# Optimization experiments

Hardware: AMD Instinct MI355X
Metric: run time of the kernel (lower is better)

Reference implementation:

```python
import jax, jax.numpy as jnp
import numpy as np

B, H, S, HD = 4, 16, 4096, 64
DIM = 2 * HD
NF = 9
LAMBDA_INIT = 0.01


def setup_inputs() -> dict:
    key = jax.random.key(0)
    ks = jax.random.split(key, 8)
    shape = (B, H, S, HD)
    Q_t = jax.random.normal(ks[0], shape, jnp.float32)
    Q_prime_t = jax.random.normal(ks[1], shape, jnp.float32)
    K_t = jax.random.normal(ks[2], shape, jnp.float32)
    K_prime_t = jax.random.normal(ks[3], shape, jnp.float32)
    V = jax.random.normal(ks[4], shape, jnp.float32)
    lambdas = jnp.full((NF,), LAMBDA_INIT, jnp.float32)
    # xavier_uniform for [NF, DIM] linear weights
    bound = float(np.sqrt(6.0 / (NF + DIM)))
    Wq = jax.random.uniform(ks[5], (NF, DIM), jnp.float32, -bound, bound)
    Wk = jax.random.uniform(ks[6], (NF, DIM), jnp.float32, -bound, bound)
    return {"Q_t": Q_t, "Q_prime_t": Q_prime_t, "K_t": K_t,
            "K_prime_t": K_prime_t, "V": V,
            "lambdas": lambdas, "Wq": Wq, "Wk": Wk}


def _ste_argmax_route(scores):
    # forward: hard one-hot; backward: softmax gradient (straight-through)
    idx = jnp.argmax(scores, axis=-1)
    one_hot = jax.nn.one_hot(idx, scores.shape[-1], dtype=scores.dtype)
    soft = jax.nn.softmax(scores, axis=-1)
    return one_hot + soft - jax.lax.stop_gradient(soft)


def _lambda_for(x, x_prime, W, lambdas):
    cat = jax.lax.stop_gradient(jnp.concatenate([x, x_prime], axis=-1))  # [B,H,S,2hd]
    scores = jnp.einsum('bshd,nd->bshn'.replace('s', 'x'), cat, W)  # placeholder
    return scores


def reference(Q_t, Q_prime_t, K_t, K_prime_t, V, lambdas, Wq, Wk):
    # routing scores (routers see detached inputs)
    Q_cat = jax.lax.stop_gradient(jnp.concatenate([Q_t, Q_prime_t], axis=-1))  # [B,H,S,2hd]
    K_cat = jax.lax.stop_gradient(jnp.concatenate([K_t, K_prime_t], axis=-1))
    q_scores = jnp.einsum('bhsd,nd->bhsn', Q_cat, Wq)
    k_scores = jnp.einsum('bhsd,nd->bhsn', K_cat, Wk)
    q_route = _ste_argmax_route(q_scores)  # [B,H,S,NF]
    k_route = _ste_argmax_route(k_scores)
    lambda_q = jnp.sum(q_route * lambdas, axis=-1, keepdims=True)  # [B,H,S,1]
    lambda_k = jnp.sum(k_route * lambdas, axis=-1, keepdims=True)
    Q_diff = Q_t - lambda_q * Q_prime_t
    K_diff = K_t - lambda_k * K_prime_t
    KV = jnp.einsum('bhsd,bhse->bhde', K_diff, V)   # [B,H,hd,hd]
    O = jnp.einsum('bhsd,bhde->bhse', Q_diff, KV)   # [B,H,S,hd]
    return O
```

## Files before the change

kernel.cpp:

```cpp
#include <hip/hip_runtime.h>


#define Sx 4096
#define HDx 64
#define NF 9
#define NHEAD 64
#define NCHK 32
#define SCK (Sx / NCHK)
#define NTK (SCK / 64)
#define NCHO 64
#define LROW 72

typedef __attribute__((ext_vector_type(8))) short bf16x8;
typedef __attribute__((ext_vector_type(4))) float f32x4;

__device__ __forceinline__ unsigned short f2bf(float f) {
    union { float f; unsigned u; } x; x.f = f;
    unsigned r = x.u + 0x7fffu + ((x.u >> 16) & 1u);
    return (unsigned short)(r >> 16);
}
__device__ __forceinline__ float bf2f(unsigned short b) {
    union { unsigned u; float f; } x; x.u = ((unsigned)b) << 16;
    return x.f;
}
__device__ __forceinline__ bf16x8 pack8(float4 a, float4 b) {
    bf16x8 r;
    r[0] = (short)f2bf(a.x); r[1] = (short)f2bf(a.y);
    r[2] = (short)f2bf(a.z); r[3] = (short)f2bf(a.w);
    r[4] = (short)f2bf(b.x); r[5] = (short)f2bf(b.y);
    r[6] = (short)f2bf(b.z); r[7] = (short)f2bf(b.w);
    return r;
}

__device__ __forceinline__ float route_lam(float v, int l15, const float* lam9) {
    int idx = l15;
#pragma unroll
    for (int m = 1; m < 16; m <<= 1) {
        float ov = __shfl_xor(v, m, 16);
        int   oi = __shfl_xor(idx, m, 16);
        bool take = (ov > v) || (ov == v && oi < idx);
        v = take ? ov : v; idx = take ? oi : idx;
    }
    return lam9[idx];
}

__device__ __forceinline__ float lam_bcast(float r0, float r1, float r2, float r3, int l15) {
    const int src = ((l15 >> 2) << 4) + l15;
    float t0 = __shfl(r0, src);
    float t1 = __shfl(r1, src);
    float t2 = __shfl(r2, src);
    float t3 = __shfl(r3, src);
    float lo = (l15 & 1) ? t1 : t0;
    float hi = (l15 & 1) ? t3 : t2;
    return (l15 & 2) ? hi : lo;
}

__global__ __launch_bounds__(256, 4) void kv_kernel(
    const float* __restrict__ Kt, const float* __restrict__ Kp,
    const float* __restrict__ V,  const float* __restrict__ lambdas,
    const float* __restrict__ Wk, float* __restrict__ KVt)
{
    __shared__ __align__(16) unsigned short kd_s[64][LROW];
    __shared__ float lam9[16];

    const int tid  = threadIdx.x;
    const int lane = tid & 63;
    const int wave = tid >> 6;
    const int l15  = lane & 15;
    const int q    = lane >> 4;
    const int head  = blockIdx.x & (NHEAD - 1);
    const int chunk = blockIdx.x >> 6;
    const size_t hbase = (size_t)head * Sx * HDx;
    const int sbase = chunk * SCK;
    const int myrow = wave * 16 + l15;

    if (tid < NF) lam9[tid] = lambdas[tid];

    bf16x8 wb[4];
#pragma unroll
    for (int h = 0; h < 4; ++h)
#pragma unroll
        for (int j = 0; j < 8; ++j) {
            float w = (l15 < NF) ? Wk[l15 * 128 + h * 32 + q * 8 + j] : 0.f;
            wb[h][j] = (short)f2bf(w);
        }

    f32x4 acc[4];
#pragma unroll
    for (int mt = 0; mt < 4; ++mt) acc[mt] = (f32x4){0.f, 0.f, 0.f, 0.f};

    const float* kt0 = Kt + hbase + (size_t)(sbase + myrow) * HDx + q * 8;
    const float* kp0 = Kp + hbase + (size_t)(sbase + myrow) * HDx + q * 8;
    float4 a0 = *(const float4*)(kt0),      a1 = *(const float4*)(kt0 + 4);
    float4 a2 = *(const float4*)(kt0 + 32), a3 = *(const float4*)(kt0 + 36);
    float4 b0 = *(const float4*)(kp0),      b1 = *(const float4*)(kp0 + 4);
    float4 b2 = *(const float4*)(kp0 + 32), b3 = *(const float4*)(kp0 + 36);
    float vv[16];
#pragma unroll
    for (int h = 0; h < 2; ++h)
#pragma unroll
        for (int j = 0; j < 8; ++j)
            vv[h * 8 + j] = V[hbase + (size_t)(sbase + h * 32 + q * 8 + j) * HDx + wave * 16 + l15];

    __syncthreads();

    bf16x8 af[4];
    af[0] = pack8(a0, a1); af[1] = pack8(a2, a3);
    af[2] = pack8(b0, b1); af[3] = pack8(b2, b3);

#pragma unroll
    for (int t = 0; t < NTK; ++t) {
        f32x4 sc = (f32x4){0.f, 0.f, 0.f, 0.f};
#pragma unroll
        for (int h = 0; h < 4; ++h)
            sc = __builtin_amdgcn_mfma_f32_16x16x32_bf16(af[h], wb[h], sc, 0, 0, 0);
        float lr0 = route_lam((l15 < NF) ? sc[0] : -3.4e38f, l15, lam9);
        float lr1 = route_lam((l15 < NF) ? sc[1] : -3.4e38f, l15, lam9);
        float lr2 = route_lam((l15 < NF) ? sc[2] : -3.4e38f, l15, lam9);
        float lr3 = route_lam((l15 < NF) ? sc[3] : -3.4e38f, l15, lam9);
        const float lam = lam_bcast(lr0, lr1, lr2, lr3, l15);

#pragma unroll
        for (int h = 0; h < 2; ++h)
#pragma unroll
            for (int j = 0; j < 8; ++j)
                kd_s[h * 32 + q * 8 + j][myrow] =
                    f2bf(bf2f((unsigned short)af[h][j]) - lam * bf2f((unsigned short)af[2 + h][j]));

        float4 na0, na1, na2, na3, nb0, nb1, nb2, nb3;
        float nvv[16];
        if (t + 1 < NTK) {
            const int s0n = sbase + (t + 1) * 64;
            const float* ktn = Kt + hbase + (size_t)(s0n + myrow) * HDx + q * 8;
            const float* kpn = Kp + hbase + (size_t)(s0n + myrow) * HDx + q * 8;
            na0 = *(const float4*)(ktn);      na1 = *(const float4*)(ktn + 4);
            na2 = *(const float4*)(ktn + 32); na3 = *(const float4*)(ktn + 36);
            nb0 = *(const float4*)(kpn);      nb1 = *(const float4*)(kpn + 4);
            nb2 = *(const float4*)(kpn + 32); nb3 = *(const float4*)(kpn + 36);
#pragma unroll
            for (int h = 0; h < 2; ++h)
#pragma unroll
                for (int j = 0; j < 8; ++j)
                    nvv[h * 8 + j] = V[hbase + (size_t)(s0n + h * 32 + q * 8 + j) * HDx + wave * 16 + l15];
        }

        bf16x8 bv[2];
#pragma unroll
        for (int h = 0; h < 2; ++h)
#pragma unroll
            for (int j = 0; j < 8; ++j) bv[h][j] = (short)f2bf(vv[h * 8 + j]);

        __syncthreads();

#pragma unroll
        for (int h = 0; h < 2; ++h)
#pragma unroll
            for (int mt = 0; mt < 4; ++mt) {
                bf16x8 ad = *(const bf16x8*)&kd_s[mt * 16 + l15][h * 32 + q * 8];
                acc[mt] = __builtin_amdgcn_mfma_f32_16x16x32_bf16(ad, bv[h], acc[mt], 0, 0, 0);
            }

        if (t + 1 < NTK) {
            __syncthreads();
            af[0] = pack8(na0, na1); af[1] = pack8(na2, na3);
            af[2] = pack8(nb0, nb1); af[3] = pack8(nb2, nb3);
#pragma unroll
            for (int j = 0; j < 16; ++j) vv[j] = nvv[j];
        }
    }

    float* kvh = KVt + head * (HDx * HDx);
#pragma unroll
    for (int mt = 0; mt < 4; ++mt)
#pragma unroll
        for (int r = 0; r < 4; ++r) {
            const int d = mt * 16 + q * 4 + r;
            const int e = wave * 16 + l15;
            atomicAdd(&kvh[e * 64 + d], acc[mt][r]);
        }
}

__global__ __launch_bounds__(256, 4) void out_kernel(
    const float* __restrict__ Qt, const float* __restrict__ Qp,
    const float* __restrict__ lambdas, const float* __restrict__ Wq,
    const float* __restrict__ KVt, float* __restrict__ O)
{
    __shared__ float lam9[16];

    const int tid  = threadIdx.x;
    const int lane = tid & 63;
    const int wave = tid >> 6;
    const int l15  = lane & 15;
    const int q    = lane >> 4;
    const int head  = blockIdx.x & (NHEAD - 1);
    const int chunk = blockIdx.x >> 6;
    const size_t hbase = (size_t)head * Sx * HDx;
    const int s0 = chunk * 64;
    const int myrow = wave * 16 + l15;

    if (tid < NF) lam9[tid] = lambdas[tid];

    const float* qt0 = Qt + hbase + (size_t)(s0 + myrow) * HDx + q * 8;
    const float* qp0 = Qp + hbase + (size_t)(s0 + myrow) * HDx + q * 8;
    float4 a0 = *(const float4*)(qt0),      a1 = *(const float4*)(qt0 + 4);
    float4 a2 = *(const float4*)(qt0 + 32), a3 = *(const float4*)(qt0 + 36);
    float4 b0 = *(const float4*)(qp0),      b1 = *(const float4*)(qp0 + 4);
    float4 b2 = *(const float4*)(qp0 + 32), b3 = *(const float4*)(qp0 + 36);

    bf16x8 wb[4];
#pragma unroll
    for (int h = 0; h < 4; ++h)
#pragma unroll
        for (int j = 0; j < 8; ++j) {
            float w = (l15 < NF) ? Wq[l15 * 128 + h * 32 + q * 8 + j] : 0.f;
            wb[h][j] = (short)f2bf(w);
        }

    bf16x8 bkv[4][2];
    const float* kvh = KVt + head * (HDx * HDx);
#pragma unroll
    for (int nt = 0; nt < 4; ++nt)
#pragma unroll
        for (int h = 0; h < 2; ++h) {
            const float* p = &kvh[(nt * 16 + l15) * 64 + h * 32 + q * 8];
            bkv[nt][h] = pack8(*(const float4*)p, *(const float4*)(p + 4));
        }

    __syncthreads();

    bf16x8 af[4];
    af[0] = pack8(a0, a1); af[1] = pack8(a2, a3);
    af[2] = pack8(b0, b1); af[3] = pack8(b2, b3);

    f32x4 sc = (f32x4){0.f, 0.f, 0.f, 0.f};
#pragma unroll
    for (int h = 0; h < 4; ++h)
        sc = __builtin_amdgcn_mfma_f32_16x16x32_bf16(af[h], wb[h], sc, 0, 0, 0);
    float lr0 = route_lam((l15 < NF) ? sc[0] : -3.4e38f, l15, lam9);
    float lr1 = route_lam((l15 < NF) ? sc[1] : -3.4e38f, l15, lam9);
    float lr2 = route_lam((l15 < NF) ? sc[2] : -3.4e38f, l15, lam9);
    float lr3 = route_lam((l15 < NF) ? sc[3] : -3.4e38f, l15, lam9);
    const float lam = lam_bcast(lr0, lr1, lr2, lr3, l15);

    bf16x8 ad[2];
#pragma unroll
    for (int h = 0; h < 2; ++h)
#pragma unroll
        for (int j = 0; j < 8; ++j)
            ad[h][j] = (short)f2bf(bf2f((unsigned short)af[h][j])
                                   - lam * bf2f((unsigned short)af[2 + h][j]));

    f32x4 oacc[4];
#pragma unroll
    for (int nt = 0; nt < 4; ++nt) oacc[nt] = (f32x4){0.f, 0.f, 0.f, 0.f};
#pragma unroll
    for (int h = 0; h < 2; ++h)
#pragma unroll
        for (int nt = 0; nt < 4; ++nt)
            oacc[nt] = __builtin_amdgcn_mfma_f32_16x16x32_bf16(ad[h], bkv[nt][h], oacc[nt], 0, 0, 0);

#pragma unroll
    for (int nt = 0; nt < 4; ++nt)
#pragma unroll
        for (int r = 0; r < 4; ++r) {
            const int row = s0 + wave * 16 + q * 4 + r;
            O[hbase + (size_t)row * HDx + nt * 16 + l15] = oacc[nt][r];
        }
}

extern "C" void kernel_launch(void* const* d_in, const int* in_sizes, int n_in,
                              void* d_out, int out_size, void* d_ws, size_t ws_size,
                              hipStream_t stream) {
    const float* Qt      = (const float*)d_in[0];
    const float* Qp      = (const float*)d_in[1];
    const float* Kt      = (const float*)d_in[2];
    const float* Kp      = (const float*)d_in[3];
    const float* V       = (const float*)d_in[4];
    const float* lambdas = (const float*)d_in[5];
    const float* Wq      = (const float*)d_in[6];
    const float* Wk      = (const float*)d_in[7];
    float* O  = (float*)d_out;
    float* KV = (float*)d_ws;

    hipMemsetAsync(d_ws, 0, (size_t)NHEAD * HDx * HDx * sizeof(float), stream);
    kv_kernel <<<NHEAD * NCHK, 256, 0, stream>>>(Kt, Kp, V, lambdas, Wk, KV);
    out_kernel<<<NHEAD * NCHO, 256, 0, stream>>>(Qt, Qp, lambdas, Wq, KV, O);
}
```

Measured before the change: 417.7 us.

## Replace atomic KV accumulation with partial slots, reduction kernel, and bf16 KV

The KV pass now writes per-chunk partial KV matrices to workspace, and a separate reduce kernel sums them and stores KV as bf16. This replaces the memset plus global atomics. The out kernel reads the bf16 KV directly and processes two 64-row tiles per block. The KV kernel drops its manual register prefetch in favour of a double-buffered shared tile. The change adds a kernel launch and extra workspace traffic, and it falls back to the atomic path when workspace is small.

```diff
diff --git a/kernel.cpp b/kernel.cpp
--- a/kernel.cpp
+++ b/kernel.cpp
@@ -5,10 +5,9 @@
 #define HDx 64
 #define NF 9
 #define NHEAD 64
-#define NCHK 32
-#define SCK (Sx / NCHK)
-#define NTK (SCK / 64)
-#define NCHO 64
+#define NCHO 32
+#define SCO (Sx / NCHO)
+#define NTO (SCO / 64)
 #define LROW 72
 
 typedef __attribute__((ext_vector_type(8))) short bf16x8;
@@ -55,12 +54,13 @@
     return (l15 & 2) ? hi : lo;
 }
 
+template<int PARTIAL>
 __global__ __launch_bounds__(256, 4) void kv_kernel(
     const float* __restrict__ Kt, const float* __restrict__ Kp,
     const float* __restrict__ V,  const float* __restrict__ lambdas,
-    const float* __restrict__ Wk, float* __restrict__ KVt)
+    const float* __restrict__ Wk, float* __restrict__ KVout, int nchk)
 {
-    __shared__ __align__(16) unsigned short kd_s[64][LROW];
+    __shared__ __align__(16) unsigned short kd_s[2][64][LROW];
     __shared__ float lam9[16];
 
     const int tid  = threadIdx.x;
@@ -71,7 +71,9 @@
     const int head  = blockIdx.x & (NHEAD - 1);
     const int chunk = blockIdx.x >> 6;
     const size_t hbase = (size_t)head * Sx * HDx;
-    const int sbase = chunk * SCK;
+    const int sck   = Sx / nchk;
+    const int ntk   = sck >> 6;
+    const int sbase = chunk * sck;
     const int myrow = wave * 16 + l15;
 
     if (tid < NF) lam9[tid] = lambdas[tid];
@@ -89,27 +91,27 @@
 #pragma unroll
     for (int mt = 0; mt < 4; ++mt) acc[mt] = (f32x4){0.f, 0.f, 0.f, 0.f};
 
-    const float* kt0 = Kt + hbase + (size_t)(sbase + myrow) * HDx + q * 8;
-    const float* kp0 = Kp + hbase + (size_t)(sbase + myrow) * HDx + q * 8;
-    float4 a0 = *(const float4*)(kt0),      a1 = *(const float4*)(kt0 + 4);
-    float4 a2 = *(const float4*)(kt0 + 32), a3 = *(const float4*)(kt0 + 36);
-    float4 b0 = *(const float4*)(kp0),      b1 = *(const float4*)(kp0 + 4);
-    float4 b2 = *(const float4*)(kp0 + 32), b3 = *(const float4*)(kp0 + 36);
-    float vv[16];
-#pragma unroll
-    for (int h = 0; h < 2; ++h)
-#pragma unroll
-        for (int j = 0; j < 8; ++j)
-            vv[h * 8 + j] = V[hbase + (size_t)(sbase + h * 32 + q * 8 + j) * HDx + wave * 16 + l15];
-
     __syncthreads();
 
-    bf16x8 af[4];
-    af[0] = pack8(a0, a1); af[1] = pack8(a2, a3);
-    af[2] = pack8(b0, b1); af[3] = pack8(b2, b3);
-
-#pragma unroll
-    for (int t = 0; t < NTK; ++t) {
+    for (int t = 0; t < ntk; ++t) {
+        const int s0 = sbase + t * 64;
+        const float* kt0 = Kt + hbase + (size_t)(s0 + myrow) * HDx + q * 8;
+        const float* kp0 = Kp + hbase + (size_t)(s0 + myrow) * HDx + q * 8;
+        float4 a0 = *(const float4*)(kt0),      a1 = *(const float4*)(kt0 + 4);
+        float4 a2 = *(const float4*)(kt0 + 32), a3 = *(const float4*)(kt0 + 36);
+        float4 b0 = *(const float4*)(kp0),      b1 = *(const float4*)(kp0 + 4);
+        float4 b2 = *(const float4*)(kp0 + 32), b3 = *(const float4*)(kp0 + 36);
+        float vv[16];
+#pragma unroll
+        for (int h = 0; h < 2; ++h)
+#pragma unroll
+            for (int j = 0; j < 8; ++j)
+                vv[h * 8 + j] = V[hbase + (size_t)(s0 + h * 32 + q * 8 + j) * HDx + wave * 16 + l15];
+
+        bf16x8 af[4];
+        af[0] = pack8(a0, a1); af[1] = pack8(a2, a3);
+        af[2] = pack8(b0, b1); af[3] = pack8(b2, b3);
+
         f32x4 sc = (f32x4){0.f, 0.f, 0.f, 0.f};
 #pragma unroll
         for (int h = 0; h < 4; ++h)
@@ -124,26 +126,9 @@
         for (int h = 0; h < 2; ++h)
 #pragma unroll
             for (int j = 0; j < 8; ++j)
-                kd_s[h * 32 + q * 8 + j][myrow] =
+                kd_s[t & 1][h * 32 + q * 8 + j][myrow] =
                     f2bf(bf2f((unsigned short)af[h][j]) - lam * bf2f((unsigned short)af[2 + h][j]));
 
-        float4 na0, na1, na2, na3, nb0, nb1, nb2, nb3;
-        float nvv[16];
-        if (t + 1 < NTK) {
-            const int s0n = sbase + (t + 1) * 64;
-            const float* ktn = Kt + hbase + (size_t)(s0n + myrow) * HDx + q * 8;
-            const float* kpn = Kp + hbase + (size_t)(s0n + myrow) * HDx + q * 8;
-            na0 = *(const float4*)(ktn);      na1 = *(const float4*)(ktn + 4);
-            na2 = *(const float4*)(ktn + 32); na3 = *(const float4*)(ktn + 36);
-            nb0 = *(const float4*)(kpn);      nb1 = *(const float4*)(kpn + 4);
-            nb2 = *(const float4*)(kpn + 32); nb3 = *(const float4*)(kpn + 36);
-#pragma unroll
-            for (int h = 0; h < 2; ++h)
-#pragma unroll
-                for (int j = 0; j < 8; ++j)
-                    nvv[h * 8 + j] = V[hbase + (size_t)(s0n + h * 32 + q * 8 + j) * HDx + wave * 16 + l15];
-        }
-
         bf16x8 bv[2];
 #pragma unroll
         for (int h = 0; h < 2; ++h)
@@ -156,34 +141,58 @@
         for (int h = 0; h < 2; ++h)
 #pragma unroll
             for (int mt = 0; mt < 4; ++mt) {
-                bf16x8 ad = *(const bf16x8*)&kd_s[mt * 16 + l15][h * 32 + q * 8];
+                bf16x8 ad = *(const bf16x8*)&kd_s[t & 1][mt * 16 + l15][h * 32 + q * 8];
                 acc[mt] = __builtin_amdgcn_mfma_f32_16x16x32_bf16(ad, bv[h], acc[mt], 0, 0, 0);
             }
-
-        if (t + 1 < NTK) {
-            __syncthreads();
-            af[0] = pack8(na0, na1); af[1] = pack8(na2, na3);
-            af[2] = pack8(nb0, nb1); af[3] = pack8(nb2, nb3);
-#pragma unroll
-            for (int j = 0; j < 16; ++j) vv[j] = nvv[j];
+    }
+
+    if (PARTIAL) {
+        float* slot = KVout + (size_t)(head * nchk + chunk) * (HDx * HDx);
+#pragma unroll
+        for (int mt = 0; mt < 4; ++mt)
+#pragma unroll
+            for (int r = 0; r < 4; ++r)
+                slot[(mt * 16 + q * 4 + r) * 64 + wave * 16 + l15] = acc[mt][r];
+    } else {
+        float* kvh = KVout + head * (HDx * HDx);
+#pragma unroll
+        for (int mt = 0; mt < 4; ++mt)
+#pragma unroll
+            for (int r = 0; r < 4; ++r)
+                atomicAdd(&kvh[(wave * 16 + l15) * 64 + mt * 16 + q * 4 + r], acc[mt][r]);
+    }
+}
+
+__global__ __launch_bounds__(256) void kv_reduce(
+    const float* __restrict__ P, unsigned short* __restrict__ KVB, int nchk)
+{
+    const int head = blockIdx.x;
+    const int d  = threadIdx.x & 63;
+    const int eq = threadIdx.x >> 6;
+    const float* base = P + (size_t)head * nchk * (HDx * HDx) + d * 64 + eq * 16;
+    float s[16];
+#pragma unroll
+    for (int i = 0; i < 16; ++i) s[i] = 0.f;
+    for (int p = 0; p < nchk; ++p) {
+        const float4* q4 = (const float4*)(base + (size_t)p * (HDx * HDx));
+#pragma unroll
+        for (int k = 0; k < 4; ++k) {
+            float4 v = q4[k];
+            s[4 * k + 0] += v.x; s[4 * k + 1] += v.y;
+            s[4 * k + 2] += v.z; s[4 * k + 3] += v.w;
         }
     }
-
-    float* kvh = KVt + head * (HDx * HDx);
-#pragma unroll
-    for (int mt = 0; mt < 4; ++mt)
-#pragma unroll
-        for (int r = 0; r < 4; ++r) {
-            const int d = mt * 16 + q * 4 + r;
-            const int e = wave * 16 + l15;
-            atomicAdd(&kvh[e * 64 + d], acc[mt][r]);
-        }
-}
-
+    unsigned short* o = KVB + (size_t)head * (HDx * HDx) + d;
+#pragma unroll
+    for (int i = 0; i < 16; ++i)
+        o[(eq * 16 + i) * 64] = f2bf(s[i]);
+}
+
+template<int BF>
 __global__ __launch_bounds__(256, 4) void out_kernel(
     const float* __restrict__ Qt, const float* __restrict__ Qp,
     const float* __restrict__ lambdas, const float* __restrict__ Wq,
-    const float* __restrict__ KVt, float* __restrict__ O)
+    const void* __restrict__ KV, float* __restrict__ O)
 {
     __shared__ float lam9[16];
 
@@ -195,17 +204,10 @@
     const int head  = blockIdx.x & (NHEAD - 1);
     const int chunk = blockIdx.x >> 6;
     const size_t hbase = (size_t)head * Sx * HDx;
-    const int s0 = chunk * 64;
+    const int s00 = chunk * SCO;
     const int myrow = wave * 16 + l15;
 
     if (tid < NF) lam9[tid] = lambdas[tid];
-
-    const float* qt0 = Qt + hbase + (size_t)(s0 + myrow) * HDx + q * 8;
-    const float* qp0 = Qp + hbase + (size_t)(s0 + myrow) * HDx + q * 8;
-    float4 a0 = *(const float4*)(qt0),      a1 = *(const float4*)(qt0 + 4);
-    float4 a2 = *(const float4*)(qt0 + 32), a3 = *(const float4*)(qt0 + 36);
-    float4 b0 = *(const float4*)(qp0),      b1 = *(const float4*)(qp0 + 4);
-    float4 b2 = *(const float4*)(qp0 + 32), b3 = *(const float4*)(qp0 + 36);
 
     bf16x8 wb[4];
 #pragma unroll
@@ -217,55 +219,74 @@
         }
 
     bf16x8 bkv[4][2];
-    const float* kvh = KVt + head * (HDx * HDx);
-#pragma unroll
-    for (int nt = 0; nt < 4; ++nt)
-#pragma unroll
-        for (int h = 0; h < 2; ++h) {
-            const float* p = &kvh[(nt * 16 + l15) * 64 + h * 32 + q * 8];
-            bkv[nt][h] = pack8(*(const float4*)p, *(const float4*)(p + 4));
-        }
+    if (BF) {
+        const unsigned short* kvb = (const unsigned short*)KV + (size_t)head * (HDx * HDx);
+#pragma unroll
+        for (int nt = 0; nt < 4; ++nt)
+#pragma unroll
+            for (int h = 0; h < 2; ++h)
+                bkv[nt][h] = *(const bf16x8*)&kvb[(nt * 16 + l15) * 64 + h * 32 + q * 8];
+    } else {
+        const float* kvh = (const float*)KV + (size_t)head * (HDx * HDx);
+#pragma unroll
+        for (int nt = 0; nt < 4; ++nt)
+#pragma unroll
+            for (int h = 0; h < 2; ++h) {
+                const float* p = &kvh[(nt * 16 + l15) * 64 + h * 32 + q * 8];
+                bkv[nt][h] = pack8(*(const float4*)p, *(const float4*)(p + 4));
+            }
+    }
 
     __syncthreads();
 
-    bf16x8 af[4];
-    af[0] = pack8(a0, a1); af[1] = pack8(a2, a3);
-    af[2] = pack8(b0, b1); af[3] = pack8(b2, b3);
-
-    f32x4 sc = (f32x4){0.f, 0.f, 0.f, 0.f};
-#pragma unroll
-    for (int h = 0; h < 4; ++h)
-        sc = __builtin_amdgcn_mfma_f32_16x16x32_bf16(af[h], wb[h], sc, 0, 0, 0);
-    float lr0 = route_lam((l15 < NF) ? sc[0] : -3.4e38f, l15, lam9);
-    float lr1 = route_lam((l15 < NF) ? sc[1] : -3.4e38f, l15, lam9);
-    float lr2 = route_lam((l15 < NF) ? sc[2] : -3.4e38f, l15, lam9);
-    float lr3 = route_lam((l15 < NF) ? sc[3] : -3.4e38f, l15, lam9);
-    const float lam = lam_bcast(lr0, lr1, lr2, lr3, l15);
-
-    bf16x8 ad[2];
-#pragma unroll
-    for (int h = 0; h < 2; ++h)
-#pragma unroll
-        for (int j = 0; j < 8; ++j)
-            ad[h][j] = (short)f2bf(bf2f((unsigned short)af[h][j])
-                                   - lam * bf2f((unsigned short)af[2 + h][j]));
-
-    f32x4 oacc[4];
-#pragma unroll
-    for (int nt = 0; nt < 4; ++nt) oacc[nt] = (f32x4){0.f, 0.f, 0.f, 0.f};
-#pragma unroll
-    for (int h = 0; h < 2; ++h)
+    for (int t = 0; t < NTO; ++t) {
+        const int s0 = s00 + t * 64;
+        const float* qt0 = Qt + hbase + (size_t)(s0 + myrow) * HDx + q * 8;
+        const float* qp0 = Qp + hbase + (size_t)(s0 + myrow) * HDx + q * 8;
+        float4 a0 = *(const float4*)(qt0),      a1 = *(const float4*)(qt0 + 4);
+        float4 a2 = *(const float4*)(qt0 + 32), a3 = *(const float4*)(qt0 + 36);
+        float4 b0 = *(const float4*)(qp0),      b1 = *(const float4*)(qp0 + 4);
+        float4 b2 = *(const float4*)(qp0 + 32), b3 = *(const float4*)(qp0 + 36);
+
+        bf16x8 af[4];
+        af[0] = pack8(a0, a1); af[1] = pack8(a2, a3);
+        af[2] = pack8(b0, b1); af[3] = pack8(b2, b3);
+
+        f32x4 sc = (f32x4){0.f, 0.f, 0.f, 0.f};
+#pragma unroll
+        for (int h = 0; h < 4; ++h)
+            sc = __builtin_amdgcn_mfma_f32_16x16x32_bf16(af[h], wb[h], sc, 0, 0, 0);
+        float lr0 = route_lam((l15 < NF) ? sc[0] : -3.4e38f, l15, lam9);
+        float lr1 = route_lam((l15 < NF) ? sc[1] : -3.4e38f, l15, lam9);
+        float lr2 = route_lam((l15 < NF) ? sc[2] : -3.4e38f, l15, lam9);
+        float lr3 = route_lam((l15 < NF) ? sc[3] : -3.4e38f, l15, lam9);
+        const float lam = lam_bcast(lr0, lr1, lr2, lr3, l15);
+
+        bf16x8 ad[2];
+#pragma unroll
+        for (int h = 0; h < 2; ++h)
+#pragma unroll
+            for (int j = 0; j < 8; ++j)
+                ad[h][j] = (short)f2bf(bf2f((unsigned short)af[h][j])
+                                       - lam * bf2f((unsigned short)af[2 + h][j]));
+
+        f32x4 oacc[4];
+#pragma unroll
+        for (int nt = 0; nt < 4; ++nt) oacc[nt] = (f32x4){0.f, 0.f, 0.f, 0.f};
+#pragma unroll
+        for (int h = 0; h < 2; ++h)
+#pragma unroll
+            for (int nt = 0; nt < 4; ++nt)
+                oacc[nt] = __builtin_amdgcn_mfma_f32_16x16x32_bf16(ad[h], bkv[nt][h], oacc[nt], 0, 0, 0);
+
 #pragma unroll
         for (int nt = 0; nt < 4; ++nt)
-            oacc[nt] = __builtin_amdgcn_mfma_f32_16x16x32_bf16(ad[h], bkv[nt][h], oacc[nt], 0, 0, 0);
-
-#pragma unroll
-    for (int nt = 0; nt < 4; ++nt)
-#pragma unroll
-        for (int r = 0; r < 4; ++r) {
-            const int row = s0 + wave * 16 + q * 4 + r;
-            O[hbase + (size_t)row * HDx + nt * 16 + l15] = oacc[nt][r];
-        }
+#pragma unroll
+            for (int r = 0; r < 4; ++r) {
+                const int row = s0 + wave * 16 + q * 4 + r;
+                O[hbase + (size_t)row * HDx + nt * 16 + l15] = oacc[nt][r];
+            }
+    }
 }
 
 extern "C" void kernel_launch(void* const* d_in, const int* in_sizes, int n_in,
@@ -279,10 +300,24 @@
     const float* lambdas = (const float*)d_in[5];
     const float* Wq      = (const float*)d_in[6];
     const float* Wk      = (const float*)d_in[7];
-    float* O  = (float*)d_out;
-    float* KV = (float*)d_ws;
-
-    hipMemsetAsync(d_ws, 0, (size_t)NHEAD * HDx * HDx * sizeof(float), stream);
-    kv_kernel <<<NHEAD * NCHK, 256, 0, stream>>>(Kt, Kp, V, lambdas, Wk, KV);
-    out_kernel<<<NHEAD * NCHO, 256, 0, stream>>>(Qt, Qp, lambdas, Wq, KV, O);
-}
+    float* O = (float*)d_out;
+
+    const size_t KVB_RES = 1u << 20;
+    const size_t SLOT    = (size_t)HDx * HDx * sizeof(float);
+
+    int nchk = 32;
+    while (nchk > 2 && ws_size < KVB_RES + (size_t)NHEAD * nchk * SLOT) nchk >>= 1;
+
+    if (ws_size >= KVB_RES + (size_t)NHEAD * nchk * SLOT) {
+        unsigned short* KVB = (unsigned short*)d_ws;
+        float* KVP = (float*)((char*)d_ws + KVB_RES);
+        kv_kernel<1><<<NHEAD * nchk, 256, 0, stream>>>(Kt, Kp, V, lambdas, Wk, KVP, nchk);
+        kv_reduce  <<<NHEAD, 256, 0, stream>>>(KVP, KVB, nchk);
+        out_kernel<1><<<NHEAD * NCHO, 256, 0, stream>>>(Qt, Qp, lambdas, Wq, KVB, O);
+    } else {
+        float* KVf = (float*)d_ws;
+        hipMemsetAsync(d_ws, 0, (size_t)NHEAD * HDx * HDx * sizeof(float), stream);
+        kv_kernel<0><<<NHEAD * 16, 256, 0, stream>>>(Kt, Kp, V, lambdas, Wk, KVf, 16);
+        out_kernel<0><<<NHEAD * NCHO, 256, 0, stream>>>(Qt, Qp, lambdas, Wq, KVf, O);
+    }
+}
```

Result: faster. 374.4 us (-10.4%).
